# Performance work log

Hardware: AMD Instinct MI355X
Metric: run time of the kernel (lower is better)

## Reference

```python
import jax, jax.numpy as jnp
import numpy as np

WS = 8  # window_size

def conv2d(x, w, b, padding=0, dilation=1, groups=1):
    out = jax.lax.conv_general_dilated(
        x, w, window_strides=(1, 1),
        padding=[(padding, padding), (padding, padding)],
        rhs_dilation=(dilation, dilation),
        feature_group_count=groups)
    return out + b[None, :, None, None]

def lrelu(x):
    return jnp.where(x >= 0, x, 0.1 * x)

def ln_cf(x, w, b, eps=1e-6):
    # LayerNorm, channels_first: normalize over channel dim per pixel
    u = x.mean(1, keepdims=True)
    s = ((x - u) ** 2).mean(1, keepdims=True)
    x = (x - u) / jnp.sqrt(s + eps)
    return w[None, :, None, None] * x + b[None, :, None, None]

def window_part(x, ws):
    # b c (h dh) (w dw) -> b (h w) (dh dw c)
    b, c, H, W = x.shape
    h, w = H // ws, W // ws
    x = x.reshape(b, c, h, ws, w, ws).transpose(0, 2, 4, 3, 5, 1)
    return x.reshape(b, h * w, ws * ws * c)

def window_rev(x, ws, H, W, c):
    # b (h w) (dh dw c) -> b c (h dh) (w dw)
    b = x.shape[0]
    h, w = H // ws, W // ws
    x = x.reshape(b, h, w, ws, ws, c).transpose(0, 5, 1, 3, 2, 4)
    return x.reshape(b, c, H, W)

def setup_inputs() -> dict:
    key = jax.random.key(0)
    B, C, H, W = 4, 64, 256, 256
    ws = WS
    E = ws * ws * C  # 4096
    ks = iter(jax.random.split(key, 40))
    def rn(shape, scale=1.0):
        return jax.random.normal(next(ks), shape, jnp.float32) * scale
    z = lambda *s: jnp.zeros(s, jnp.float32)
    d = {}
    d['x'] = rn((B, C, H, W))
    d['Wv'] = rn((C, C, 1, 1), C ** -0.5); d['bv'] = z(C)
    d['Wri'] = rn((C // 4, C, 1, 1), C ** -0.5); d['bri'] = z(C // 4)
    d['Wrc'] = rn((C // 4, C, 1, 1), C ** -0.5); d['brc'] = z(C // 4)
    d['ln_w'] = jnp.ones((C // 4,), jnp.float32); d['ln_b'] = z(C // 4)
    d['Wca'] = rn((C, C // 4, 1, 1), (C // 4) ** -0.5); d['bca'] = z(C)
    d['Wsa'] = rn((1, C // 4, 3, 3), (9 * C // 4) ** -0.5); d['bsa'] = z(1)
    d['Wm1'] = rn((E // 2, E), E ** -0.5); d['bm1'] = z(E // 2)
    d['Wm2'] = rn((E, E // 2), (E // 2) ** -0.5); d['bm2'] = z(E)
    d['Wq'] = rn((C, C), C ** -0.5); d['bq'] = z(C)
    d['Wk'] = rn((C, C), C ** -0.5); d['bk'] = z(C)
    d['Wd1'] = rn((C, 1, 3, 3), 1.0 / 3.0); d['bd1'] = z(C)
    d['Wd2'] = rn((C, 1, 3, 3), 1.0 / 3.0); d['bd2'] = z(C)
    d['Wo'] = rn((C, C, 1, 1), C ** -0.5); d['bo'] = z(C)
    return d

def reference(x, Wv, bv, Wri, bri, Wrc, brc, ln_w, ln_b, Wca, bca, Wsa, bsa,
              Wm1, bm1, Wm2, bm2, Wq, bq, Wk, bk, Wd1, bd1, Wd2, bd2, Wo, bo):
    B, C, H, W = x.shape
    ws = WS
    E = ws * ws * C
    v = conv2d(x, Wv, bv)
    # ---- MaskPre (route) ----
    x1 = lrelu(conv2d(v, Wri, bri))                       # [B,C/4,H,W]
    x_ = lrelu(ln_cf(conv2d(v, Wrc, brc), ln_w, ln_b))    # [B,C/4,H,W]
    ca = jax.nn.sigmoid(conv2d(x_.mean((2, 3), keepdims=True), Wca, bca))  # [B,C,1,1]
    sa = jax.nn.sigmoid(conv2d(x_, Wsa, bsa, padding=1))                   # [B,1,H,W]
    xm = window_part(x1.mean(1, keepdims=True), ws)       # [B,N,ws^2]
    var_x = jnp.var(xm, axis=-1, ddof=1)                  # torch.var is unbiased
    N = var_x.shape[1]
    k_top = N // 2
    _, idx = jax.lax.top_k(-var_x, k_top)                 # k smallest-variance windows
    mask_bin = jnp.ones((B, N), x.dtype).at[jnp.arange(B)[:, None], idx].set(0.0)
    m = jnp.broadcast_to(mask_bin[:, :, None], (B, N, E))
    m = lrelu(m @ Wm1.T + bm1)
    mask = m @ Wm2.T + bm2                                # [B,N,E]
    # ---- windowed attention / skip split ----
    vs = v * sa
    vw = window_part(v, ws)                               # [B,N,ws^2*C]
    vsw = window_part(vs, ws)
    qkw = window_part(jnp.concatenate([x, x], axis=1), ws)  # [B,N,ws^2*2C]
    v1 = vw * mask
    v2 = vsw * (1.0 - mask)
    mask_qk = jnp.concatenate(
        [mask.reshape(B, N, ws * ws, C)] * 2, axis=-1).reshape(B, N, ws * ws * 2 * C)
    qk1 = (qkw * mask_qk).reshape(B, N * ws * ws, 2 * C)
    q1 = (qk1[..., :C] @ Wq.T + bq).reshape(B * N, ws * ws, C)
    k1 = (qk1[..., C:] @ Wk.T + bk).reshape(B * N, ws * ws, C)
    v1r = v1.reshape(B * N, ws * ws, C)
    attn = jax.nn.softmax(q1 @ jnp.swapaxes(k1, -1, -2), axis=-1)  # [BN,ws^2,ws^2]
    f_attn = (attn @ v1r).reshape(B, N, ws * ws * C)
    attn_out = f_attn + v2
    out = window_rev(attn_out, ws, H, W, C)               # [B,C,H,W]
    # ---- spatial conv branch + projections ----
    c1 = conv2d(out, Wd1, bd1, padding=1, groups=C)
    c2 = conv2d(c1, Wd2, bd2, padding=2, dilation=2, groups=C)
    out = jax.nn.gelu(c2, approximate=False) * ca + out
    out = conv2d(out, Wo, bo)
    return out
```

## Files before the change

kernel.cpp:

```cpp
#include <hip/hip_runtime.h>
#include <hip/hip_bf16.h>
#include <math.h>

typedef __attribute__((ext_vector_type(8))) short short8;
typedef __attribute__((ext_vector_type(16))) float f32x16;

__device__ __forceinline__ float lrelu(float x){ return x >= 0.f ? x : 0.1f*x; }
__device__ __forceinline__ float sigmoidf(float x){ return 1.f/(1.f+expf(-x)); }
__device__ __forceinline__ short f2bf(float f){
  __hip_bfloat16 hb = __float2bfloat16(f);
  return *reinterpret_cast<short*>(&hb);
}
__device__ __forceinline__ float bf16f(short s){
  return __uint_as_float(((unsigned)(unsigned short)s)<<16);
}

__device__ __forceinline__ int WFofs(int w,int part,int mt,int kt){
  return (((w*2+part)*2+mt)*4+kt)*512;
}

__global__ void k0_combine(const float* __restrict__ Wv, const float* __restrict__ bv,
                           const float* __restrict__ Wri, const float* __restrict__ bri,
                           const float* __restrict__ Wrc, const float* __restrict__ brc,
                           float* __restrict__ WriE, float* __restrict__ briE,
                           float* __restrict__ WrcE, float* __restrict__ brcE){
  int idx = blockIdx.x*256 + threadIdx.x;
  if (idx < 1024){
    int j = idx>>6, c = idx&63;
    float s1=0.f, s2=0.f;
    for (int k=0;k<64;k++){ s1 = fmaf(Wri[j*64+k], Wv[k*64+c], s1); s2 = fmaf(Wrc[j*64+k], Wv[k*64+c], s2); }
    WriE[idx]=s1; WrcE[idx]=s2;
  }
  if (idx < 16){
    float s1=bri[idx], s2=brc[idx];
    for (int k=0;k<64;k++){ s1 = fmaf(Wri[idx*64+k], bv[k], s1); s2 = fmaf(Wrc[idx*64+k], bv[k], s2); }
    briE[idx]=s1; brcE[idx]=s2;
  }
}

__global__ void k_prep(const float* __restrict__ Wq, const float* __restrict__ Wk,
                       const float* __restrict__ Wo, const float* __restrict__ Wv,
                       const float* __restrict__ WriE, const float* __restrict__ WrcE,
                       short* __restrict__ WFrag){
  int idx = blockIdx.x*256 + threadIdx.x;
  if (idx < 6144){
    int w = idx>>10, rem = idx&1023;
    int part = rem>>9, mt = (rem>>8)&1, kt = (rem>>6)&3, lane = rem&63;
    int hh = lane>>5;
    short8 frag;
    #pragma unroll
    for (int i=0;i<8;i++){
      int kl = (hh<<2) + (i&3) + ((i>>2)<<3);
      int kfull = (kt<<4) + kl;
      float val = 0.f;
      if (w < 3){
        const float* W = (w==0)?Wq:((w==1)?Wk:Wo);
        int j = (mt<<5)|(lane&31);
        val = W[j*64 + kfull];
      } else if (mt == 0){
        int j = lane&31;
        if (w==3)      val = Wv[j*64 + kfull];
        else if (w==4) val = Wv[(32+j)*64 + kfull];
        else           val = (j<16) ? WriE[j*64 + kfull] : WrcE[(j-16)*64 + kfull];
      }
      short hi = f2bf(val);
      frag[i] = part ? f2bf(val - bf16f(hi)) : hi;
    }
    *(short8*)&WFrag[WFofs(w,part,mt,kt) + (lane<<3)] = frag;
  }
}

__global__ void k_premask1(const float* __restrict__ Wm1, const float* __restrict__ bm1,
                           float* __restrict__ mrow1, float* __restrict__ mrow0){
  __shared__ float red[256];
  int j = blockIdx.x, tid = threadIdx.x;
  const float* row = Wm1 + (size_t)j*4096;
  float s=0.f;
  for (int e=tid;e<4096;e+=256) s += row[e];
  red[tid]=s; __syncthreads();
  for (int o=128;o;o>>=1){ if (tid<o) red[tid]+=red[tid+o]; __syncthreads(); }
  if (tid==0){
    float t = red[0]+bm1[j];
    mrow1[j] = lrelu(t);
    mrow0[j] = lrelu(bm1[j]);
  }
}

__global__ void k_premask2(const float* __restrict__ Wm2, const float* __restrict__ bm2,
                           const float* __restrict__ mrow1, const float* __restrict__ mrow0,
                           float* __restrict__ mask1, float* __restrict__ mask0,
                           float* __restrict__ mask1T, float* __restrict__ mask0T){
  __shared__ float r1[256], r0[256];
  int e = blockIdx.x, tid = threadIdx.x;
  const float* row = Wm2 + (size_t)e*2048;
  float s1=0.f, s0=0.f;
  for (int j=tid;j<2048;j+=256){ float wv=row[j]; s1 = fmaf(wv, mrow1[j], s1); s0 = fmaf(wv, mrow0[j], s0); }
  r1[tid]=s1; r0[tid]=s0; __syncthreads();
  for (int o=128;o;o>>=1){ if (tid<o){ r1[tid]+=r1[tid+o]; r0[tid]+=r0[tid+o]; } __syncthreads(); }
  if (tid==0){
    float m1 = r1[0]+bm2[e], m0 = r0[0]+bm2[e];
    mask1[e]=m1; mask0[e]=m0;
    int p = e>>6, c = e&63;
    mask1T[(c<<6)|p]=m1; mask0T[(c<<6)|p]=m0;
  }
}

__global__ __launch_bounds__(256, 4) void k1_pw(
    const float* __restrict__ x, const short* __restrict__ WFrag,
    const float* __restrict__ bv,
    const float* __restrict__ briE, const float* __restrict__ brcE,
    const float* __restrict__ ln_w, const float* __restrict__ ln_b,
    float* __restrict__ v_w, float* __restrict__ x_, float* __restrict__ xm,
    float* __restrict__ bsum){
  __shared__ float wred[4][16];
  int tid = threadIdx.x, lane = tid&63, wvi = tid>>6, l31 = lane&31, h = lane>>5;
  int blk = blockIdx.x;
  int wid = (blk<<1) | (wvi>>1);
  int ht  = wvi & 1;
  int b = wid >> 10, n = wid & 1023;
  int pix0 = ((n>>5)<<11) | ((n&31)<<3);
  int p = (ht<<5) | l31;
  int hw = pix0 + ((p>>3)<<8) + (p&7);
  size_t xb = (((size_t)b)<<22) + hw;
  int nb = wid << 12;
  short8 XH[4], XL[4];
  #pragma unroll
  for (int kt=0;kt<4;kt++){
    float xv[8];
    #pragma unroll
    for (int i=0;i<8;i++){
      int c = (kt<<4) + (h<<2) + (i&3) + ((i>>2)<<3);
      xv[i] = x[xb + ((size_t)c<<16)];
    }
    short8 fh, fl;
    #pragma unroll
    for (int i=0;i<8;i++){ short hi=f2bf(xv[i]); fh[i]=hi; fl[i]=f2bf(xv[i]-bf16f(hi)); }
    XH[kt]=fh; XL[kt]=fl;
  }
  f32x16 T[3];
  #pragma unroll
  for (int t3=0;t3<3;t3++){
    f32x16 acc;
    #pragma unroll
    for (int r=0;r<16;r++) acc[r]=0.f;
    #pragma unroll
    for (int kt=0;kt<4;kt++){
      short8 WAh = *(const short8*)&WFrag[WFofs(3+t3,0,0,kt) + (lane<<3)];
      short8 WAl = *(const short8*)&WFrag[WFofs(3+t3,1,0,kt) + (lane<<3)];
      acc = __builtin_amdgcn_mfma_f32_32x32x16_bf16(WAh, XH[kt], acc, 0,0,0);
      acc = __builtin_amdgcn_mfma_f32_32x32x16_bf16(WAh, XL[kt], acc, 0,0,0);
      acc = __builtin_amdgcn_mfma_f32_32x32x16_bf16(WAl, XH[kt], acc, 0,0,0);
    }
    T[t3]=acc;
  }
  #pragma unroll
  for (int r=0;r<16;r++){
    int c0 = (r&3) + ((r>>2)<<3) + (h<<2);
    v_w[nb + (c0<<6) + p]        = T[0][r] + bv[c0];
    v_w[nb + ((c0+32)<<6) + p]   = T[1][r] + bv[c0+32];
  }
  float s1 = 0.f;
  #pragma unroll
  for (int r=0;r<8;r++){
    int j = (r&3) + ((r>>2)<<3) + (h<<2);
    s1 += lrelu(T[2][r] + briE[j]);
  }
  s1 += __shfl_xor(s1, 32);
  xm[(((size_t)b)<<16) + hw] = s1*(1.f/16.f);
  float vals[8], u = 0.f;
  #pragma unroll
  for (int r=0;r<8;r++){
    int j = (r&3) + ((r>>2)<<3) + (h<<2);
    float t = T[2][8+r] + brcE[j];
    vals[r]=t; u += t;
  }
  u += __shfl_xor(u, 32);
  u *= (1.f/16.f);
  float s2 = 0.f;
  #pragma unroll
  for (int r=0;r<8;r++){ float d = vals[r]-u; s2 += d*d; }
  s2 += __shfl_xor(s2, 32);
  float inv = 1.0f / sqrtf(s2*(1.f/16.f) + 1e-6f);
  float bs[8];
  #pragma unroll
  for (int r=0;r<8;r++){
    int j = (r&3) + ((r>>2)<<3) + (h<<2);
    float t = lrelu((vals[r]-u)*inv*ln_w[j] + ln_b[j]);
    x_[(((size_t)(b*16+j))<<16) + hw] = t;
    bs[r]=t;
  }
  #pragma unroll
  for (int r=0;r<8;r++){
    float val = bs[r];
    val += __shfl_xor(val,1); val += __shfl_xor(val,2); val += __shfl_xor(val,4);
    val += __shfl_xor(val,8); val += __shfl_xor(val,16);
    bs[r]=val;
  }
  if (l31==0){
    #pragma unroll
    for (int r=0;r<8;r++){
      int j = (r&3) + ((r>>2)<<3) + (h<<2);
      wred[wvi][j] = bs[r];
    }
  }
  __syncthreads();
  if (tid<16) bsum[blk*16+tid] = wred[0][tid]+wred[1][tid]+wred[2][tid]+wred[3][tid];
}

__global__ __launch_bounds__(256) void k2_sa(const float* __restrict__ x_,
    const float* __restrict__ Wsa, const float* __restrict__ bsa, float* __restrict__ sa){
  int idx = blockIdx.x*256 + threadIdx.x;
  int b = idx>>16; int hw = idx & 65535; int h = hw>>8, wcol = hw & 255;
  float acc = bsa[0];
  for (int ch=0; ch<16; ++ch){
    const float* plane = x_ + (((size_t)(b*16+ch))<<16);
    #pragma unroll
    for (int ky=0;ky<3;ky++){
      int y = h + ky - 1;
      if ((unsigned)y >= 256u) continue;
      #pragma unroll
      for (int kx=0;kx<3;kx++){
        int xx = wcol + kx - 1;
        if ((unsigned)xx >= 256u) continue;
        acc = fmaf(Wsa[ch*9+ky*3+kx], plane[(y<<8)+xx], acc);
      }
    }
  }
  sa[idx] = sigmoidf(acc);
}

__global__ void k3_ca(const float* __restrict__ bsum, const float* __restrict__ Wca,
                      const float* __restrict__ bca, float* __restrict__ ca){
  __shared__ float meanx[4][16];
  int tid = threadIdx.x;
  if (tid < 64){
    int b = tid>>4, j = tid&15;
    float s=0.f;
    for (int blk=0;blk<512;blk++) s += bsum[(b*512+blk)*16 + j];
    meanx[b][j] = s*(1.f/65536.f);
  }
  __syncthreads();
  int b = tid>>6, oc = tid&63;
  float a = bca[oc];
  #pragma unroll
  for (int j=0;j<16;j++) a = fmaf(Wca[oc*16+j], meanx[b][j], a);
  ca[tid] = sigmoidf(a);
}

__global__ void k4a_var(const float* __restrict__ xm, float* __restrict__ var){
  int t = blockIdx.x*256 + threadIdx.x;
  int b = t>>10, n = t&1023, wh = n>>5, ww = n&31;
  const float* base = xm + (((size_t)b)<<16) + (wh<<11) + (ww<<3);
  float s=0.f;
  #pragma unroll
  for (int dh=0;dh<8;dh++){
    #pragma unroll
    for (int dw=0;dw<8;dw++) s += base[(dh<<8)+dw];
  }
  float mean = s*(1.f/64.f);
  float ss=0.f;
  #pragma unroll
  for (int dh=0;dh<8;dh++){
    #pragma unroll
    for (int dw=0;dw<8;dw++){ float d = base[(dh<<8)+dw]-mean; ss += d*d; }
  }
  var[t] = ss*(1.f/63.f);
}

__global__ __launch_bounds__(1024) void k4b_sel(const float* __restrict__ var, float* __restrict__ sel){
  __shared__ float vs[1024];
  int b = blockIdx.x, tid = threadIdx.x;
  float mine = var[b*1024+tid];
  vs[tid]=mine; __syncthreads();
  int rank=0;
  for (int j=0;j<1024;j++){
    float o = vs[j];
    rank += (o < mine) || (o == mine && j < tid);
  }
  sel[b*1024+tid] = (rank >= 512) ? 1.f : 0.f;
}

__global__ __launch_bounds__(256, 3) void k6_attn(
    const float* __restrict__ x, const float* __restrict__ v_w, const float* __restrict__ sa,
    const float* __restrict__ sel,
    const float* __restrict__ mask1, const float* __restrict__ mask0,
    const float* __restrict__ mask1T, const float* __restrict__ mask0T,
    const short* __restrict__ WFrag,
    const float* __restrict__ bq, const float* __restrict__ bk,
    float* __restrict__ out){
  __shared__ short8 KAlds[2][2][8][64];
  int tid = threadIdx.x;
  int lane = tid & 63, wvi = tid >> 6;
  int wi = wvi >> 1, ht = wvi & 1;
  int l31 = lane & 31, h = lane >> 5;
  int bid = blockIdx.x;
  int blk = ((bid & 7) << 8) | (bid >> 3);
  int wg = (blk << 1) | wi;
  int b = wg >> 10, n = wg & 1023;
  int pix0 = ((n >> 5) << 11) | ((n & 31) << 3);
  bool sel1 = sel[wg] > 0.5f;
  const float* mrow  = sel1 ? mask1  : mask0;
  const float* mrowT = sel1 ? mask1T : mask0T;
  size_t cbase = (((size_t)b) << 22) + pix0;
  int nb = wg << 12;

  int p = (ht<<5) | l31;
  int po = ((p>>3)<<8) | (p&7);
  size_t gp = cbase + po;
  const float* mr = mrow + (p<<6);
  short8 XBh[4], XBl[4];
  #pragma unroll
  for (int kt=0;kt<4;kt++){
    float4 ma = *(const float4*)&mr[(kt<<4)+(h<<2)];
    float4 mb = *(const float4*)&mr[(kt<<4)+(h<<2)+8];
    float xv[8];
    #pragma unroll
    for (int i=0;i<8;i++){
      int c = (kt<<4) + (h<<2) + (i&3) + ((i>>2)<<3);
      xv[i] = x[gp + ((size_t)c<<16)];
    }
    xv[0]*=ma.x; xv[1]*=ma.y; xv[2]*=ma.z; xv[3]*=ma.w;
    xv[4]*=mb.x; xv[5]*=mb.y; xv[6]*=mb.z; xv[7]*=mb.w;
    short8 fh, fl;
    #pragma unroll
    for (int i=0;i<8;i++){
      short hi = f2bf(xv[i]); fh[i]=hi; fl[i]=f2bf(xv[i]-bf16f(hi));
    }
    XBh[kt]=fh; XBl[kt]=fl;
  }

  short8 QBh[4], QBl[4];
  #pragma unroll
  for (int mt=0;mt<2;mt++){
    f32x16 acc;
    #pragma unroll
    for (int r=0;r<16;r++) acc[r]=0.f;
    #pragma unroll
    for (int kt=0;kt<4;kt++){
      short8 WAh = *(const short8*)&WFrag[WFofs(0,0,mt,kt) + (lane<<3)];
      short8 WAl = *(const short8*)&WFrag[WFofs(0,1,mt,kt) + (lane<<3)];
      acc = __builtin_amdgcn_mfma_f32_32x32x16_bf16(WAh, XBh[kt], acc, 0,0,0);
      acc = __builtin_amdgcn_mfma_f32_32x32x16_bf16(WAh, XBl[kt], acc, 0,0,0);
      acc = __builtin_amdgcn_mfma_f32_32x32x16_bf16(WAl, XBh[kt], acc, 0,0,0);
    }
    #pragma unroll
    for (int rr=0;rr<4;rr++){
      float4 b4 = *(const float4*)&bq[(mt<<5)+(rr<<3)+(h<<2)];
      acc[4*rr+0]+=b4.x; acc[4*rr+1]+=b4.y; acc[4*rr+2]+=b4.z; acc[4*rr+3]+=b4.w;
    }
    #pragma unroll
    for (int kk=0;kk<2;kk++){
      short8 fh, fl;
      #pragma unroll
      for (int i=0;i<8;i++){
        float vv = acc[8*kk+i];
        short hi = f2bf(vv); fh[i]=hi; fl[i]=f2bf(vv-bf16f(hi));
      }
      QBh[2*mt+kk]=fh; QBl[2*mt+kk]=fl;
    }
  }

  #pragma unroll
  for (int mt=0;mt<2;mt++){
    f32x16 acc;
    #pragma unroll
    for (int r=0;r<16;r++) acc[r]=0.f;
    #pragma unroll
    for (int kt=0;kt<4;kt++){
      short8 WAh = *(const short8*)&WFrag[WFofs(1,0,mt,kt) + (lane<<3)];
      short8 WAl = *(const short8*)&WFrag[WFofs(1,1,mt,kt) + (lane<<3)];
      acc = __builtin_amdgcn_mfma_f32_32x32x16_bf16(WAh, XBh[kt], acc, 0,0,0);
      acc = __builtin_amdgcn_mfma_f32_32x32x16_bf16(WAh, XBl[kt], acc, 0,0,0);
      acc = __builtin_amdgcn_mfma_f32_32x32x16_bf16(WAl, XBh[kt], acc, 0,0,0);
    }
    #pragma unroll
    for (int rr=0;rr<4;rr++){
      float4 b4 = *(const float4*)&bk[(mt<<5)+(rr<<3)+(h<<2)];
      acc[4*rr+0]+=b4.x; acc[4*rr+1]+=b4.y; acc[4*rr+2]+=b4.z; acc[4*rr+3]+=b4.w;
    }
    #pragma unroll
    for (int kk=0;kk<2;kk++){
      short8 fh, fl;
      #pragma unroll
      for (int i=0;i<8;i++){
        float vv = acc[8*kk+i];
        short hi = f2bf(vv); fh[i]=hi; fl[i]=f2bf(vv-bf16f(hi));
      }
      KAlds[wi][ht][2*mt+kk][lane]   = fh;
      KAlds[wi][ht][4+2*mt+kk][lane] = fl;
    }
  }
  __syncthreads();

  f32x16 ST[2];
  #pragma unroll
  for (int mt=0;mt<2;mt++){
    f32x16 acc;
    #pragma unroll
    for (int r=0;r<16;r++) acc[r]=0.f;
    #pragma unroll
    for (int kt=0;kt<4;kt++){
      short8 kh = KAlds[wi][mt][kt][lane];
      short8 kl = KAlds[wi][mt][4+kt][lane];
      acc = __builtin_amdgcn_mfma_f32_32x32x16_bf16(kh, QBh[kt], acc, 0,0,0);
      acc = __builtin_amdgcn_mfma_f32_32x32x16_bf16(kh, QBl[kt], acc, 0,0,0);
      acc = __builtin_amdgcn_mfma_f32_32x32x16_bf16(kl, QBh[kt], acc, 0,0,0);
    }
    ST[mt] = acc;
  }

  float mx = ST[0][0];
  #pragma unroll
  for (int r=1;r<16;r++) mx = fmaxf(mx, ST[0][r]);
  #pragma unroll
  for (int r=0;r<16;r++) mx = fmaxf(mx, ST[1][r]);
  mx = fmaxf(mx, __shfl_xor(mx, 32));
  float sum = 0.f;
  #pragma unroll
  for (int mt=0;mt<2;mt++)
    #pragma unroll
    for (int r=0;r<16;r++){ float e = expf(ST[mt][r]-mx); ST[mt][r]=e; sum += e; }
  sum += __shfl_xor(sum, 32);
  float inv = 1.f/sum;

  short8 PB[4];
  #pragma unroll
  for (int mt=0;mt<2;mt++)
    #pragma unroll
    for (int kk=0;kk<2;kk++){
      short8 f;
      #pragma unroll
      for (int i=0;i<8;i++) f[i] = f2bf(ST[mt][8*kk+i]*inv);
      PB[2*mt+kk]=f;
    }

  float sav = sa[(((size_t)b)<<16) + pix0 + po];

  #pragma unroll
  for (int mtc=0;mtc<2;mtc++){
    int c0 = (mtc<<5);
    int cl = c0 | l31;
    const float* vwr = v_w + nb + (cl<<6);
    const float* mTr = mrowT + (cl<<6);
    f32x16 acc;
    #pragma unroll
    for (int r=0;r<16;r++) acc[r]=0.f;
    #pragma unroll
    for (int kt=0;kt<4;kt++){
      float4 va  = *(const float4*)&vwr[(kt<<4) + (h<<2)];
      float4 vb2 = *(const float4*)&vwr[(kt<<4) + (h<<2) + 8];
      float4 ma = *(const float4*)&mTr[(kt<<4)+(h<<2)];
      float4 mb = *(const float4*)&mTr[(kt<<4)+(h<<2)+8];
      short8 f;
      f[0]=f2bf(va.x*ma.x); f[1]=f2bf(va.y*ma.y); f[2]=f2bf(va.z*ma.z); f[3]=f2bf(va.w*ma.w);
      f[4]=f2bf(vb2.x*mb.x); f[5]=f2bf(vb2.y*mb.y); f[6]=f2bf(vb2.z*mb.z); f[7]=f2bf(vb2.w*mb.w);
      acc = __builtin_amdgcn_mfma_f32_32x32x16_bf16(f, PB[kt], acc, 0,0,0);
    }
    #pragma unroll
    for (int rr=0;rr<4;rr++){
      float4 m4 = *(const float4*)&mr[c0+(rr<<3)+(h<<2)];
      #pragma unroll
      for (int t=0;t<4;t++){
        int c = c0 + (rr<<3) + (h<<2) + t;
        float vv = v_w[nb + (c<<6) + p];
        float mm = (t==0)?m4.x:(t==1)?m4.y:(t==2)?m4.z:m4.w;
        out[cbase + ((size_t)c<<16) + po] = acc[4*rr+t] + sav*vv*(1.f-mm);
      }
    }
  }
}

__global__ __launch_bounds__(256) void k7_fused(const float* __restrict__ in,
    const float* __restrict__ Wd1, const float* __restrict__ bd1,
    const float* __restrict__ Wd2, const float* __restrict__ bd2,
    const float* __restrict__ ca, float* __restrict__ dwout){
  __shared__ float IN[38*39];
  __shared__ float C1[36*37];
  int blk = blockIdx.x;
  int tile = blk & 63;
  int tx = tile & 7, ty = tile >> 3;
  int ch = (blk>>6) & 63, b = blk>>12;
  int x0 = tx<<5, y0 = ty<<5;
  const float* plane = in + (((size_t)(b*64+ch))<<16);
  int tid = threadIdx.x;
  for (int e = tid; e < 1444; e += 256){
    int r = e/38, cc = e - r*38;
    int y = y0 + r - 3, xx = x0 + cc - 3;
    float vv = 0.f;
    if ((unsigned)y < 256u && (unsigned)xx < 256u) vv = plane[(y<<8)+xx];
    IN[r*39+cc] = vv;
  }
  __syncthreads();
  float w1[9], w2[9];
  #pragma unroll
  for (int t=0;t<9;t++){ w1[t]=Wd1[ch*9+t]; w2[t]=Wd2[ch*9+t]; }
  float b1 = bd1[ch];
  for (int e = tid; e < 1296; e += 256){
    int r = e/36, cc = e - r*36;
    int yc1 = y0 + r - 2, xc1 = x0 + cc - 2;
    float acc = 0.f;
    if ((unsigned)yc1 < 256u && (unsigned)xc1 < 256u){
      acc = b1;
      #pragma unroll
      for (int ky=0;ky<3;ky++)
        #pragma unroll
        for (int kx=0;kx<3;kx++)
          acc = fmaf(w1[ky*3+kx], IN[(r+ky)*39 + cc+kx], acc);
    }
    C1[r*37+cc] = acc;
  }
  __syncthreads();
  int px = tid & 31, py0 = tid >> 5;
  float cav = ca[b*64+ch];
  float b2 = bd2[ch];
  #pragma unroll
  for (int q=0;q<4;q++){
    int py = py0 + (q<<3);
    float acc = b2;
    #pragma unroll
    for (int ky=0;ky<3;ky++)
      #pragma unroll
      for (int kx=0;kx<3;kx++)
        acc = fmaf(w2[ky*3+kx], C1[(py+2*ky)*37 + px+2*kx], acc);
    float g = 0.5f*acc*(1.f + erff(acc*0.70710678118654752f));
    float resid = IN[(py+3)*39 + px+3];
    size_t o = (((size_t)(b*64+ch))<<16) + ((size_t)((y0+py)<<8)) + x0+px;
    dwout[o] = fmaf(g, cav, resid);
  }
}

__global__ __launch_bounds__(256, 3) void k7c_proj(const float* __restrict__ in,
    const short* __restrict__ WFrag, const float* __restrict__ bo,
    float* __restrict__ out){
  int tid = threadIdx.x;
  int lane = tid & 63, wvi = tid >> 6;
  int l31 = lane & 31, h = lane >> 5;
  int blk = blockIdx.x;
  int b = blk >> 8;
  int hw0 = ((blk & 255) << 8) | (wvi << 6);
  size_t base = ((size_t)b) << 22;
  #pragma unroll
  for (int nt=0;nt<2;nt++){
    int px = hw0 | (nt<<5) | l31;
    short8 XH[4], XL[4];
    #pragma unroll
    for (int kt=0;kt<4;kt++){
      float xv[8];
      #pragma unroll
      for (int i=0;i<8;i++){
        int c = (kt<<4) + (h<<2) + (i&3) + ((i>>2)<<3);
        xv[i] = in[base + ((size_t)c<<16) + px];
      }
      short8 fh, fl;
      #pragma unroll
      for (int i=0;i<8;i++){
        short hi = f2bf(xv[i]); fh[i]=hi; fl[i]=f2bf(xv[i]-bf16f(hi));
      }
      XH[kt]=fh; XL[kt]=fl;
    }
    #pragma unroll
    for (int mt=0;mt<2;mt++){
      f32x16 acc;
      #pragma unroll
      for (int r=0;r<16;r++) acc[r]=0.f;
      #pragma unroll
      for (int kt=0;kt<4;kt++){
        short8 WAh = *(const short8*)&WFrag[WFofs(2,0,mt,kt) + (lane<<3)];
        short8 WAl = *(const short8*)&WFrag[WFofs(2,1,mt,kt) + (lane<<3)];
        acc = __builtin_amdgcn_mfma_f32_32x32x16_bf16(WAh, XH[kt], acc, 0,0,0);
        acc = __builtin_amdgcn_mfma_f32_32x32x16_bf16(WAh, XL[kt], acc, 0,0,0);
        acc = __builtin_amdgcn_mfma_f32_32x32x16_bf16(WAl, XH[kt], acc, 0,0,0);
      }
      #pragma unroll
      for (int rr=0;rr<4;rr++){
        float4 b4 = *(const float4*)&bo[(mt<<5)+(rr<<3)+(h<<2)];
        #pragma unroll
        for (int t=0;t<4;t++){
          int oc = (mt<<5) + (rr<<3) + (h<<2) + t;
          float bb = (t==0)?b4.x:(t==1)?b4.y:(t==2)?b4.z:b4.w;
          out[base + ((size_t)oc<<16) + px] = acc[4*rr+t] + bb;
        }
      }
    }
  }
}

extern "C" void kernel_launch(void* const* d_in, const int* in_sizes, int n_in,
                              void* d_out, int out_size, void* d_ws, size_t ws_size,
                              hipStream_t stream) {
  const float* x    = (const float*)d_in[0];
  const float* Wv   = (const float*)d_in[1];
  const float* bv   = (const float*)d_in[2];
  const float* Wri  = (const float*)d_in[3];
  const float* bri  = (const float*)d_in[4];
  const float* Wrc  = (const float*)d_in[5];
  const float* brc  = (const float*)d_in[6];
  const float* ln_w = (const float*)d_in[7];
  const float* ln_b = (const float*)d_in[8];
  const float* Wca  = (const float*)d_in[9];
  const float* bca  = (const float*)d_in[10];
  const float* Wsa  = (const float*)d_in[11];
  const float* bsa  = (const float*)d_in[12];
  const float* Wm1  = (const float*)d_in[13];
  const float* bm1  = (const float*)d_in[14];
  const float* Wm2  = (const float*)d_in[15];
  const float* bm2  = (const float*)d_in[16];
  const float* Wq   = (const float*)d_in[17];
  const float* bq   = (const float*)d_in[18];
  const float* Wk   = (const float*)d_in[19];
  const float* bk   = (const float*)d_in[20];
  const float* Wd1  = (const float*)d_in[21];
  const float* bd1  = (const float*)d_in[22];
  const float* Wd2  = (const float*)d_in[23];
  const float* bd2  = (const float*)d_in[24];
  const float* Wo   = (const float*)d_in[25];
  const float* bo   = (const float*)d_in[26];
  float* out = (float*)d_out;

  float* ws = (float*)d_ws;
  float* v_buf   = ws;
  float* out_buf = v_buf + 16777216;
  float* x_buf   = out_buf + 16777216;
  float* xm_buf  = x_buf + 4194304;
  float* sa_buf  = xm_buf + 262144;
  float* bsum    = sa_buf + 262144;
  float* ca_buf  = bsum + 32768;
  float* var_buf = ca_buf + 256;
  float* sel_buf = var_buf + 4096;
  float* mrow1   = sel_buf + 4096;
  float* mrow0   = mrow1 + 2048;
  float* mask1   = mrow0 + 2048;
  float* mask0   = mask1 + 4096;
  float* mask1T  = mask0 + 4096;
  float* mask0T  = mask1T + 4096;
  float* WriE    = mask0T + 4096;
  float* WrcE    = WriE + 1024;
  float* briE    = WrcE + 1024;
  float* brcE    = briE + 16;
  short* WFrag   = (short*)(brcE + 16);
  float* dw_buf  = v_buf;

  k0_combine<<<4,256,0,stream>>>(Wv,bv,Wri,bri,Wrc,brc,WriE,briE,WrcE,brcE);
  k_prep<<<24,256,0,stream>>>(Wq,Wk,Wo,Wv,WriE,WrcE,WFrag);
  k_premask1<<<2048,256,0,stream>>>(Wm1,bm1,mrow1,mrow0);
  k_premask2<<<4096,256,0,stream>>>(Wm2,bm2,mrow1,mrow0,mask1,mask0,mask1T,mask0T);
  k1_pw<<<2048,256,0,stream>>>(x,WFrag,bv,briE,brcE,ln_w,ln_b,v_buf,x_buf,xm_buf,bsum);
  k2_sa<<<1024,256,0,stream>>>(x_buf,Wsa,bsa,sa_buf);
  k3_ca<<<1,256,0,stream>>>(bsum,Wca,bca,ca_buf);
  k4a_var<<<16,256,0,stream>>>(xm_buf,var_buf);
  k4b_sel<<<4,1024,0,stream>>>(var_buf,sel_buf);
  k6_attn<<<2048,256,0,stream>>>(x,v_buf,sa_buf,sel_buf,mask1,mask0,mask1T,mask0T,WFrag,bq,bk,out_buf);
  k7_fused<<<16384,256,0,stream>>>(out_buf,Wd1,bd1,Wd2,bd2,ca_buf,dw_buf);
  k7c_proj<<<1024,256,0,stream>>>(dw_buf,WFrag,bo,out);
}
```

Measured before the change: 367.2 us.

## Coalesce k1 loads by row-major pixels, tile k2 conv in LDS, shrink k6 blocks

k1_pw now assigns pixels to lanes in row-major order, so x reads are contiguous along image rows, and it scatters the v output into the windowed layout instead. k2_sa stages a 16x16 tile plus halo for all 16 channels in shared memory before computing the 3x3 conv, which removes repeated global loads. k6_attn is split into 128-thread blocks, one window each, with doubled grid size and a higher occupancy hint. The window-layout v writes become strided, and k2 spends time on LDS staging and a block-wide sync.

```diff
diff --git a/kernel.cpp b/kernel.cpp
--- a/kernel.cpp
+++ b/kernel.cpp
@@ -115,14 +115,11 @@
   __shared__ float wred[4][16];
   int tid = threadIdx.x, lane = tid&63, wvi = tid>>6, l31 = lane&31, h = lane>>5;
   int blk = blockIdx.x;
-  int wid = (blk<<1) | (wvi>>1);
-  int ht  = wvi & 1;
-  int b = wid >> 10, n = wid & 1023;
-  int pix0 = ((n>>5)<<11) | ((n&31)<<3);
-  int p = (ht<<5) | l31;
-  int hw = pix0 + ((p>>3)<<8) + (p&7);
+  int b = blk>>9;
+  int hw = ((blk&511)<<7) | (wvi<<5) | l31;
   size_t xb = (((size_t)b)<<22) + hw;
-  int nb = wid << 12;
+  int row = hw>>8, col = hw&255;
+  int vbase = (((b<<10) | ((row>>3)<<5) | (col>>3))<<12) + (((row&7)<<3) | (col&7));
   short8 XH[4], XL[4];
   #pragma unroll
   for (int kt=0;kt<4;kt++){
@@ -156,8 +153,8 @@
   #pragma unroll
   for (int r=0;r<16;r++){
     int c0 = (r&3) + ((r>>2)<<3) + (h<<2);
-    v_w[nb + (c0<<6) + p]        = T[0][r] + bv[c0];
-    v_w[nb + ((c0+32)<<6) + p]   = T[1][r] + bv[c0+32];
+    v_w[vbase + (c0<<6)]      = T[0][r] + bv[c0];
+    v_w[vbase + ((c0+32)<<6)] = T[1][r] + bv[c0+32];
   }
   float s1 = 0.f;
   #pragma unroll
@@ -209,24 +206,32 @@
 
 __global__ __launch_bounds__(256) void k2_sa(const float* __restrict__ x_,
     const float* __restrict__ Wsa, const float* __restrict__ bsa, float* __restrict__ sa){
-  int idx = blockIdx.x*256 + threadIdx.x;
-  int b = idx>>16; int hw = idx & 65535; int h = hw>>8, wcol = hw & 255;
+  __shared__ float T[16*324];
+  int blk = blockIdx.x;
+  int b = blk>>8;
+  int tile = blk&255;
+  int x0 = (tile&15)<<4, y0 = (tile>>4)<<4;
+  int tid = threadIdx.x;
+  for (int e=tid; e<5184; e+=256){
+    int ch = e/324, rem = e-ch*324, r = rem/18, cc = rem-r*18;
+    int y = y0+r-1, xx = x0+cc-1;
+    float v = 0.f;
+    if ((unsigned)y<256u && (unsigned)xx<256u) v = x_[(((size_t)(b*16+ch))<<16)+(y<<8)+xx];
+    T[e] = v;
+  }
+  __syncthreads();
+  int px = tid&15, py = tid>>4;
   float acc = bsa[0];
-  for (int ch=0; ch<16; ++ch){
-    const float* plane = x_ + (((size_t)(b*16+ch))<<16);
-    #pragma unroll
-    for (int ky=0;ky<3;ky++){
-      int y = h + ky - 1;
-      if ((unsigned)y >= 256u) continue;
-      #pragma unroll
-      for (int kx=0;kx<3;kx++){
-        int xx = wcol + kx - 1;
-        if ((unsigned)xx >= 256u) continue;
-        acc = fmaf(Wsa[ch*9+ky*3+kx], plane[(y<<8)+xx], acc);
-      }
-    }
-  }
-  sa[idx] = sigmoidf(acc);
+  #pragma unroll
+  for (int ch=0; ch<16; ch++){
+    const float* Tc = T + ch*324 + py*18 + px;
+    #pragma unroll
+    for (int ky=0;ky<3;ky++)
+      #pragma unroll
+      for (int kx=0;kx<3;kx++)
+        acc = fmaf(Wsa[ch*9+ky*3+kx], Tc[ky*18+kx], acc);
+  }
+  sa[(((size_t)b)<<16) + ((y0+py)<<8) + x0+px] = sigmoidf(acc);
 }
 
 __global__ void k3_ca(const float* __restrict__ bsum, const float* __restrict__ Wca,
@@ -280,7 +285,7 @@
   sel[b*1024+tid] = (rank >= 512) ? 1.f : 0.f;
 }
 
-__global__ __launch_bounds__(256, 3) void k6_attn(
+__global__ __launch_bounds__(128, 5) void k6_attn(
     const float* __restrict__ x, const float* __restrict__ v_w, const float* __restrict__ sa,
     const float* __restrict__ sel,
     const float* __restrict__ mask1, const float* __restrict__ mask0,
@@ -288,14 +293,12 @@
     const short* __restrict__ WFrag,
     const float* __restrict__ bq, const float* __restrict__ bk,
     float* __restrict__ out){
-  __shared__ short8 KAlds[2][2][8][64];
+  __shared__ short8 KAlds[2][8][64];
   int tid = threadIdx.x;
-  int lane = tid & 63, wvi = tid >> 6;
-  int wi = wvi >> 1, ht = wvi & 1;
+  int lane = tid & 63, ht = tid >> 6;
   int l31 = lane & 31, h = lane >> 5;
   int bid = blockIdx.x;
-  int blk = ((bid & 7) << 8) | (bid >> 3);
-  int wg = (blk << 1) | wi;
+  int wg = ((bid & 7) << 9) | (bid >> 3);
   int b = wg >> 10, n = wg & 1023;
   int pix0 = ((n >> 5) << 11) | ((n & 31) << 3);
   bool sel1 = sel[wg] > 0.5f;
@@ -386,8 +389,8 @@
         float vv = acc[8*kk+i];
         short hi = f2bf(vv); fh[i]=hi; fl[i]=f2bf(vv-bf16f(hi));
       }
-      KAlds[wi][ht][2*mt+kk][lane]   = fh;
-      KAlds[wi][ht][4+2*mt+kk][lane] = fl;
+      KAlds[ht][2*mt+kk][lane]   = fh;
+      KAlds[ht][4+2*mt+kk][lane] = fl;
     }
   }
   __syncthreads();
@@ -400,8 +403,8 @@
     for (int r=0;r<16;r++) acc[r]=0.f;
     #pragma unroll
     for (int kt=0;kt<4;kt++){
-      short8 kh = KAlds[wi][mt][kt][lane];
-      short8 kl = KAlds[wi][mt][4+kt][lane];
+      short8 kh = KAlds[mt][kt][lane];
+      short8 kl = KAlds[mt][4+kt][lane];
       acc = __builtin_amdgcn_mfma_f32_32x32x16_bf16(kh, QBh[kt], acc, 0,0,0);
       acc = __builtin_amdgcn_mfma_f32_32x32x16_bf16(kh, QBl[kt], acc, 0,0,0);
       acc = __builtin_amdgcn_mfma_f32_32x32x16_bf16(kl, QBh[kt], acc, 0,0,0);
@@ -649,7 +652,7 @@
   k3_ca<<<1,256,0,stream>>>(bsum,Wca,bca,ca_buf);
   k4a_var<<<16,256,0,stream>>>(xm_buf,var_buf);
   k4b_sel<<<4,1024,0,stream>>>(var_buf,sel_buf);
-  k6_attn<<<2048,256,0,stream>>>(x,v_buf,sa_buf,sel_buf,mask1,mask0,mask1T,mask0T,WFrag,bq,bk,out_buf);
+  k6_attn<<<4096,128,0,stream>>>(x,v_buf,sa_buf,sel_buf,mask1,mask0,mask1T,mask0T,WFrag,bq,bk,out_buf);
   k7_fused<<<16384,256,0,stream>>>(out_buf,Wd1,bd1,Wd2,bd2,ca_buf,dw_buf);
   k7c_proj<<<1024,256,0,stream>>>(dw_buf,WFrag,bo,out);
 }
```

New measurement: 424.4 us. +15.6%, slower.
